# Optimization experiments

Hardware: AMD Instinct MI355X
Metric: run time of the kernel (lower is better)

## Reference

```python
import jax, jax.numpy as jnp
import numpy as np

DIM = 512
N = 131072


def _linear_params(key, dim):
    # torch nn.Linear default init: U(-1/sqrt(in), 1/sqrt(in)) for W and b
    kw, kb = jax.random.split(key)
    bound = 1.0 / np.sqrt(dim)
    W = jax.random.uniform(kw, (dim, dim), jnp.float32, -bound, bound)
    b = jax.random.uniform(kb, (dim,), jnp.float32, -bound, bound)
    return W, b


def setup_inputs() -> dict:
    key = jax.random.key(0)
    ks = jax.random.split(key, 8)
    x = jax.random.normal(ks[0], (N, DIM), jnp.float32)
    h = jax.random.normal(ks[1], (N, DIM), jnp.float32)
    W_rx, b_rx = _linear_params(ks[2], DIM)
    W_rh, b_rh = _linear_params(ks[3], DIM)
    W_zx, b_zx = _linear_params(ks[4], DIM)
    W_zh, b_zh = _linear_params(ks[5], DIM)
    W_nx, b_nx = _linear_params(ks[6], DIM)
    W_nh, b_nh = _linear_params(ks[7], DIM)
    return {
        "x": x, "h": h,
        "W_rx": W_rx, "b_rx": b_rx, "W_rh": W_rh, "b_rh": b_rh,
        "W_zx": W_zx, "b_zx": b_zx, "W_zh": W_zh, "b_zh": b_zh,
        "W_nx": W_nx, "b_nx": b_nx, "W_nh": W_nh, "b_nh": b_nh,
    }


def reference(x, h, W_rx, b_rx, W_rh, b_rh, W_zx, b_zx, W_zh, b_zh,
              W_nx, b_nx, W_nh, b_nh):
    # torch Linear: y = x @ W.T + b  (W stored [out, in])
    r = jax.nn.sigmoid(x @ W_rx.T + b_rx + h @ W_rh.T + b_rh)
    z = jax.nn.sigmoid(x @ W_zx.T + b_zx + h @ W_zh.T + b_zh)
    n = jnp.tanh(x @ W_nx.T + b_nx + (r * h) @ W_nh.T + b_nh)
    return (1.0 - z) * n + z * h
```

## Files before the change

kernel.cpp:

```cpp
#include <hip/hip_runtime.h>

#define DIM 512
#define NROWS 131072

typedef __attribute__((ext_vector_type(8))) __bf16 bf16x8;
typedef __attribute__((ext_vector_type(4))) float f32x4;

__device__ __forceinline__ unsigned short f2bf(float f) {
  unsigned u = __builtin_bit_cast(unsigned, f);
  return (unsigned short)((u + 0x7FFFu + ((u >> 16) & 1u)) >> 16);
}
__device__ __forceinline__ float bf2f(unsigned short u) {
  return __builtin_bit_cast(float, (unsigned)u << 16);
}

__device__ __forceinline__ f32x4 mfma16(bf16x8 a, bf16x8 b, f32x4 c) {
  return __builtin_amdgcn_mfma_f32_16x16x32_bf16(a, b, c, 0, 0, 0);
}

__device__ __forceinline__ float sigmoid_fast(float v) {
  return 1.0f / (1.0f + __expf(-v));
}
__device__ __forceinline__ float tanh_fast(float v) {
  float e = __expf(2.0f * v);
  return 1.0f - 2.0f / (e + 1.0f);
}

__global__ void prepack_weights(const float* __restrict__ W0, const float* __restrict__ W1,
                                const float* __restrict__ W2, const float* __restrict__ W3,
                                const float* __restrict__ W4, const float* __restrict__ W5,
                                unsigned short* __restrict__ out) {
  int idx = blockIdx.x * 256 + threadIdx.x;
  int e = idx & 7;
  int l = (idx >> 3) & 63;
  int c = (idx >> 9) & 31;
  int f = (idx >> 14) & 15;
  int g = idx >> 18;
  const float* W = (g == 0) ? W0 : (g == 1) ? W1 : (g == 2) ? W2
                 : (g == 3) ? W3 : (g == 4) ? W4 : W5;
  int row = c * 16 + (l & 15);
  int kk  = f * 32 + ((l >> 4) << 3) + e;
  out[idx] = f2bf(W[row * DIM + kk]);
}

__global__ void prep_x(const float* __restrict__ x, unsigned short* __restrict__ xb) {
  size_t i = (size_t)(blockIdx.x * 256 + threadIdx.x) * 8;
  float4 a0 = *(const float4*)(x + i);
  float4 a1 = *(const float4*)(x + i + 4);
  union { unsigned short us[8]; uint4 v; } p;
  p.us[0] = f2bf(a0.x); p.us[1] = f2bf(a0.y); p.us[2] = f2bf(a0.z); p.us[3] = f2bf(a0.w);
  p.us[4] = f2bf(a1.x); p.us[5] = f2bf(a1.y); p.us[6] = f2bf(a1.z); p.us[7] = f2bf(a1.w);
  *(uint4*)(xb + i) = p.v;
}

__global__ __launch_bounds__(512, 2)
void gru_fused(const float* __restrict__ h,
               const unsigned short* __restrict__ xb,
               const unsigned char* __restrict__ WB,
               const float* __restrict__ b_rx, const float* __restrict__ b_rh,
               const float* __restrict__ b_zx, const float* __restrict__ b_zh,
               const float* __restrict__ b_nx, const float* __restrict__ b_nh,
               float* __restrict__ out) {
  __shared__ __align__(1024) unsigned char lds[65536];

  const int tid  = threadIdx.x;
  const int lane = tid & 63;
  const int w    = tid >> 6;
  const int row0 = blockIdx.x * 64;
  const int lr   = lane & 15;
  const int lk   = lane >> 4;
  const int boff = w * 4096 + lane * 16;

  auto loadB = [&](int g, int f, bf16x8 (&b)[4]) {
    const unsigned char* p = WB + (((size_t)(g * 16 + f)) << 15) + boff;
#pragma unroll
    for (int cf = 0; cf < 4; ++cf)
      b[cf] = *(const bf16x8*)(p + cf * 1024);
  };
  auto loadXA = [&](int f, bf16x8 (&a)[4]) {
#pragma unroll
    for (int rf = 0; rf < 4; ++rf)
      a[rf] = *(const bf16x8*)(xb + (size_t)(row0 + rf * 16 + lr) * DIM
                               + f * 32 + lk * 8);
  };
  auto readLDS = [&](int f, bf16x8 (&a)[4]) {
#pragma unroll
    for (int rf = 0; rf < 4; ++rf)
      a[rf] = *(const bf16x8*)&lds[f * 4096 + rf * 1024 + lane * 16];
  };

#define WINDOW(Aset, Bset, ACC)                                                \
  _Pragma("unroll")                                                            \
  for (int rf_ = 0; rf_ < 4; ++rf_)                                            \
    _Pragma("unroll")                                                          \
    for (int cf_ = 0; cf_ < 4; ++cf_)                                          \
      ACC[rf_][cf_] = mfma16(Aset[rf_], Bset[cf_], ACC[rf_][cf_]);

  bf16x8 bA[4], bB[4], xaC[4], xaN[4], ha[4];

  loadB(0, 0, bA);
  loadB(1, 0, bB);
  loadXA(0, xaC);
#pragma unroll
  for (int it = 0; it < 16; ++it) {
    int i = tid + it * 512;
    int row = i >> 7;
    int k = (i & 127) * 4;
    float4 hv4 = *(const float4*)(h + (size_t)(row0 + row) * DIM + k);
    union { unsigned short us[4]; uint2 v; } p;
    p.us[0] = f2bf(hv4.x); p.us[1] = f2bf(hv4.y);
    p.us[2] = f2bf(hv4.z); p.us[3] = f2bf(hv4.w);
    *(uint2*)&lds[(k >> 5) * 4096 + (row >> 4) * 1024
                  + (((k >> 3) & 3) * 16 + (row & 15)) * 16 + (k & 4) * 2] = p.v;
  }
  __syncthreads();

  f32x4 accR[4][4] = {}, accZ[4][4] = {};
#pragma unroll 1
  for (int f = 0; f < 16; ++f) {
    const int fn = (f < 15) ? f + 1 : 15;
    readLDS(f, ha);
    WINDOW(xaC, bA, accR);
    loadB(2, f, bA);
    WINDOW(xaC, bB, accZ);
    loadB(3, f, bB);
    loadXA(fn, xaN);
    WINDOW(ha, bA, accR);
    loadB(0, fn, bA);
    WINDOW(ha, bB, accZ);
    loadB(1, fn, bB);
#pragma unroll
    for (int rf = 0; rf < 4; ++rf) xaC[rf] = xaN[rf];
  }

  loadB(4, 0, bA);
  loadB(5, 0, bB);
  loadXA(0, xaC);
  __syncthreads();

#pragma unroll
  for (int cf = 0; cf < 4; ++cf) {
    const int col  = (w * 4 + cf) * 16 + lr;
    const float bs = b_rx[col] + b_rh[col];
    const int fcol = col >> 5;
    const int l2b  = ((col >> 3) & 3) * 16;
    const int eb   = (col & 7) * 2;
#pragma unroll
    for (int rf = 0; rf < 4; ++rf) {
#pragma unroll
      for (int j = 0; j < 4; ++j) {
        const int rsub = lk * 4 + j;
        const int addr = fcol * 4096 + rf * 1024 + (l2b + rsub) * 16 + eb;
        unsigned short hu = *(const unsigned short*)&lds[addr];
        float rv = sigmoid_fast(accR[rf][cf][j] + bs);
        *(unsigned short*)&lds[addr] = f2bf(rv * bf2f(hu));
      }
    }
  }
  __syncthreads();

  f32x4 accN[4][4] = {};
#pragma unroll 1
  for (int f = 0; f < 16; ++f) {
    const int fn = (f < 15) ? f + 1 : 15;
    readLDS(f, ha);
    WINDOW(xaC, bA, accN);
    loadB(4, fn, bA);
    loadXA(fn, xaN);
    WINDOW(ha, bB, accN);
    loadB(5, fn, bB);
#pragma unroll
    for (int rf = 0; rf < 4; ++rf) xaC[rf] = xaN[rf];
  }

#pragma unroll
  for (int cf = 0; cf < 4; ++cf) {
    const int col  = (w * 4 + cf) * 16 + lr;
    const float bn = b_nx[col] + b_nh[col];
    const float bz = b_zx[col] + b_zh[col];
#pragma unroll
    for (int rf = 0; rf < 4; ++rf) {
#pragma unroll
      for (int j = 0; j < 4; ++j) {
        const int row = rf * 16 + lk * 4 + j;
        const size_t off = (size_t)(row0 + row) * DIM + col;
        float hv = h[off];
        float nv = tanh_fast(accN[rf][cf][j] + bn);
        float zv = sigmoid_fast(accZ[rf][cf][j] + bz);
        out[off] = (1.0f - zv) * nv + zv * hv;
      }
    }
  }
#undef WINDOW
}

extern "C" void kernel_launch(void* const* d_in, const int* in_sizes, int n_in,
                              void* d_out, int out_size, void* d_ws, size_t ws_size,
                              hipStream_t stream) {
  const float* x    = (const float*)d_in[0];
  const float* h    = (const float*)d_in[1];
  const float* W_rx = (const float*)d_in[2];
  const float* b_rx = (const float*)d_in[3];
  const float* W_rh = (const float*)d_in[4];
  const float* b_rh = (const float*)d_in[5];
  const float* W_zx = (const float*)d_in[6];
  const float* b_zx = (const float*)d_in[7];
  const float* W_zh = (const float*)d_in[8];
  const float* b_zh = (const float*)d_in[9];
  const float* W_nx = (const float*)d_in[10];
  const float* b_nx = (const float*)d_in[11];
  const float* W_nh = (const float*)d_in[12];
  const float* b_nh = (const float*)d_in[13];

  unsigned char* ws = (unsigned char*)d_ws;
  unsigned short* wpack = (unsigned short*)ws;
  unsigned short* xb    = (unsigned short*)(ws + (4ull << 20));

  prepack_weights<<<6144, 256, 0, stream>>>(W_rx, W_zx, W_rh, W_zh, W_nx, W_nh, wpack);
  prep_x<<<32768, 256, 0, stream>>>(x, xb);
  gru_fused<<<NROWS / 64, 512, 0, stream>>>(h, xb, (const unsigned char*)wpack,
                                            b_rx, b_rh, b_zx, b_zh, b_nx, b_nh,
                                            (float*)d_out);
}
```

Before: 726.2 us.

## Enlarge row tile to 128 and run gates as three sequential sweeps

The fused GRU kernel now handles 128 rows per block, with 8 waves in a 2x4 grid, each computing a 64x128 output tile. The r, z and n gates are computed in three separate sweeps that share one accumulator set, with z staged through the output buffer and r*h staged in a 128 KB LDS buffer. h is optionally pre-converted to bf16 in a separate pass, and each sweep wraps its MFMAs in s_setprio. The aim is more B-operand reuse per weight load and fewer live accumulators. The cost is that x and h are re-read across sweeps, z makes an extra round trip through global memory, and the larger LDS allocation limits blocks per CU.

```diff
diff --git a/kernel.cpp b/kernel.cpp
--- a/kernel.cpp
+++ b/kernel.cpp
@@ -2,6 +2,7 @@
 
 #define DIM 512
 #define NROWS 131072
+#define MB 128
 
 typedef __attribute__((ext_vector_type(8))) __bf16 bf16x8;
 typedef __attribute__((ext_vector_type(4))) float f32x4;
@@ -43,155 +44,172 @@
   out[idx] = f2bf(W[row * DIM + kk]);
 }
 
-__global__ void prep_x(const float* __restrict__ x, unsigned short* __restrict__ xb) {
+__global__ void prep_bf16(const float* __restrict__ in, unsigned short* __restrict__ ob) {
   size_t i = (size_t)(blockIdx.x * 256 + threadIdx.x) * 8;
-  float4 a0 = *(const float4*)(x + i);
-  float4 a1 = *(const float4*)(x + i + 4);
+  float4 a0 = *(const float4*)(in + i);
+  float4 a1 = *(const float4*)(in + i + 4);
   union { unsigned short us[8]; uint4 v; } p;
   p.us[0] = f2bf(a0.x); p.us[1] = f2bf(a0.y); p.us[2] = f2bf(a0.z); p.us[3] = f2bf(a0.w);
   p.us[4] = f2bf(a1.x); p.us[5] = f2bf(a1.y); p.us[6] = f2bf(a1.z); p.us[7] = f2bf(a1.w);
-  *(uint4*)(xb + i) = p.v;
+  *(uint4*)(ob + i) = p.v;
 }
 
 __global__ __launch_bounds__(512, 2)
-void gru_fused(const float* __restrict__ h,
+void gru_fused(const float* __restrict__ x, const float* __restrict__ h,
                const unsigned short* __restrict__ xb,
+               const unsigned short* __restrict__ hb,
                const unsigned char* __restrict__ WB,
                const float* __restrict__ b_rx, const float* __restrict__ b_rh,
                const float* __restrict__ b_zx, const float* __restrict__ b_zh,
                const float* __restrict__ b_nx, const float* __restrict__ b_nh,
                float* __restrict__ out) {
-  __shared__ __align__(1024) unsigned char lds[65536];
+  __shared__ __align__(1024) unsigned char lds[131072];
 
   const int tid  = threadIdx.x;
   const int lane = tid & 63;
   const int w    = tid >> 6;
-  const int row0 = blockIdx.x * 64;
+  const int wr   = w >> 2;
+  const int wc   = w & 3;
+  const int row0 = blockIdx.x * MB;
+  const int rb   = row0 + wr * 64;
   const int lr   = lane & 15;
   const int lk   = lane >> 4;
-  const int boff = w * 4096 + lane * 16;
-
-  auto loadB = [&](int g, int f, bf16x8 (&b)[4]) {
-    const unsigned char* p = WB + (((size_t)(g * 16 + f)) << 15) + boff;
-#pragma unroll
-    for (int cf = 0; cf < 4; ++cf)
+
+  bf16x8 bX[8], bH[8], axA[4], axB[4], ahC[4];
+  f32x4 acc[4][8];
+
+  auto loadB = [&](int g, int f, bf16x8 (&b)[8]) {
+    const unsigned char* p = WB + (((size_t)(g * 16 + f)) << 15)
+                             + (wc * 8) * 1024 + lane * 16;
+#pragma unroll
+    for (int cf = 0; cf < 8; ++cf)
       b[cf] = *(const bf16x8*)(p + cf * 1024);
   };
-  auto loadXA = [&](int f, bf16x8 (&a)[4]) {
+  auto loadA = [&](const unsigned short* bp, const float* fp, int f, bf16x8 (&a)[4]) {
+    if (bp) {
+#pragma unroll
+      for (int rf = 0; rf < 4; ++rf)
+        a[rf] = *(const bf16x8*)(bp + (size_t)(rb + rf * 16 + lr) * DIM
+                                 + f * 32 + lk * 8);
+    } else {
+#pragma unroll
+      for (int rf = 0; rf < 4; ++rf) {
+        const float* p = fp + (size_t)(rb + rf * 16 + lr) * DIM + f * 32 + lk * 8;
+        float4 u0 = *(const float4*)p;
+        float4 u1 = *(const float4*)(p + 4);
+        union { unsigned short us[8]; bf16x8 v; } c;
+        c.us[0]=f2bf(u0.x); c.us[1]=f2bf(u0.y); c.us[2]=f2bf(u0.z); c.us[3]=f2bf(u0.w);
+        c.us[4]=f2bf(u1.x); c.us[5]=f2bf(u1.y); c.us[6]=f2bf(u1.z); c.us[7]=f2bf(u1.w);
+        a[rf] = c.v;
+      }
+    }
+  };
+  auto readRH = [&](int f, bf16x8 (&a)[4]) {
 #pragma unroll
     for (int rf = 0; rf < 4; ++rf)
-      a[rf] = *(const bf16x8*)(xb + (size_t)(row0 + rf * 16 + lr) * DIM
-                               + f * 32 + lk * 8);
+      a[rf] = *(const bf16x8*)&lds[f * 8192 + (wr * 4 + rf) * 1024 + lane * 16];
   };
-  auto readLDS = [&](int f, bf16x8 (&a)[4]) {
+
+#define WIN(A, B)                                                              \
+  do {                                                                         \
+    __builtin_amdgcn_s_setprio(1);                                             \
+    _Pragma("unroll")                                                          \
+    for (int rf_ = 0; rf_ < 4; ++rf_)                                          \
+      _Pragma("unroll")                                                        \
+      for (int cf_ = 0; cf_ < 8; ++cf_)                                        \
+        acc[rf_][cf_] = mfma16(A[rf_], B[cf_], acc[rf_][cf_]);                 \
+    __builtin_amdgcn_s_setprio(0);                                             \
+  } while (0)
+
+#define LOADAH_G(F)  loadA(hb, h, (F), ahC)
+#define LOADAH_RH(F) readRH((F), ahC)
+
+#define SWEEP(GX, GH, AH)                                                      \
+  {                                                                            \
+    _Pragma("unroll")                                                          \
+    for (int rf_ = 0; rf_ < 4; ++rf_)                                          \
+      _Pragma("unroll")                                                        \
+      for (int cf_ = 0; cf_ < 8; ++cf_)                                        \
+        acc[rf_][cf_] = (f32x4){0.f, 0.f, 0.f, 0.f};                           \
+    loadB((GX), 0, bX); loadB((GH), 0, bH);                                    \
+    loadA(xb, x, 0, axA); AH(0);                                               \
+    _Pragma("unroll 1")                                                        \
+    for (int f2 = 0; f2 < 8; ++f2) {                                           \
+      {                                                                        \
+        const int f1 = 2 * f2 + 1;                                             \
+        loadA(xb, x, f1, axB);                                                 \
+        WIN(axA, bX); loadB((GX), f1, bX);                                     \
+        WIN(ahC, bH); loadB((GH), f1, bH); AH(f1);                             \
+      }                                                                        \
+      {                                                                        \
+        const int f1 = (f2 < 7) ? 2 * f2 + 2 : 15;                             \
+        loadA(xb, x, f1, axA);                                                 \
+        WIN(axB, bX); loadB((GX), f1, bX);                                     \
+        WIN(ahC, bH); loadB((GH), f1, bH); AH(f1);                             \
+      }                                                                        \
+    }                                                                          \
+  }
+
+  SWEEP(1, 3, LOADAH_G);
+#pragma unroll
+  for (int cf = 0; cf < 8; ++cf) {
+    const int col = wc * 128 + cf * 16 + lr;
+    const float bz = b_zx[col] + b_zh[col];
 #pragma unroll
     for (int rf = 0; rf < 4; ++rf)
-      a[rf] = *(const bf16x8*)&lds[f * 4096 + rf * 1024 + lane * 16];
-  };
-
-#define WINDOW(Aset, Bset, ACC)                                                \
-  _Pragma("unroll")                                                            \
-  for (int rf_ = 0; rf_ < 4; ++rf_)                                            \
-    _Pragma("unroll")                                                          \
-    for (int cf_ = 0; cf_ < 4; ++cf_)                                          \
-      ACC[rf_][cf_] = mfma16(Aset[rf_], Bset[cf_], ACC[rf_][cf_]);
-
-  bf16x8 bA[4], bB[4], xaC[4], xaN[4], ha[4];
-
-  loadB(0, 0, bA);
-  loadB(1, 0, bB);
-  loadXA(0, xaC);
-#pragma unroll
-  for (int it = 0; it < 16; ++it) {
-    int i = tid + it * 512;
-    int row = i >> 7;
-    int k = (i & 127) * 4;
-    float4 hv4 = *(const float4*)(h + (size_t)(row0 + row) * DIM + k);
-    union { unsigned short us[4]; uint2 v; } p;
-    p.us[0] = f2bf(hv4.x); p.us[1] = f2bf(hv4.y);
-    p.us[2] = f2bf(hv4.z); p.us[3] = f2bf(hv4.w);
-    *(uint2*)&lds[(k >> 5) * 4096 + (row >> 4) * 1024
-                  + (((k >> 3) & 3) * 16 + (row & 15)) * 16 + (k & 4) * 2] = p.v;
-  }
-  __syncthreads();
-
-  f32x4 accR[4][4] = {}, accZ[4][4] = {};
-#pragma unroll 1
-  for (int f = 0; f < 16; ++f) {
-    const int fn = (f < 15) ? f + 1 : 15;
-    readLDS(f, ha);
-    WINDOW(xaC, bA, accR);
-    loadB(2, f, bA);
-    WINDOW(xaC, bB, accZ);
-    loadB(3, f, bB);
-    loadXA(fn, xaN);
-    WINDOW(ha, bA, accR);
-    loadB(0, fn, bA);
-    WINDOW(ha, bB, accZ);
-    loadB(1, fn, bB);
-#pragma unroll
-    for (int rf = 0; rf < 4; ++rf) xaC[rf] = xaN[rf];
-  }
-
-  loadB(4, 0, bA);
-  loadB(5, 0, bB);
-  loadXA(0, xaC);
-  __syncthreads();
-
-#pragma unroll
-  for (int cf = 0; cf < 4; ++cf) {
-    const int col  = (w * 4 + cf) * 16 + lr;
+#pragma unroll
+      for (int j = 0; j < 4; ++j) {
+        const int row = rb + rf * 16 + lk * 4 + j;
+        out[(size_t)row * DIM + col] = sigmoid_fast(acc[rf][cf][j] + bz);
+      }
+  }
+
+  SWEEP(0, 2, LOADAH_G);
+#pragma unroll
+  for (int cf = 0; cf < 8; ++cf) {
+    const int col = wc * 128 + cf * 16 + lr;
     const float bs = b_rx[col] + b_rh[col];
-    const int fcol = col >> 5;
-    const int l2b  = ((col >> 3) & 3) * 16;
-    const int eb   = (col & 7) * 2;
+    const int fI  = col >> 5;
+    const int l2b = ((col >> 3) & 3) * 16;
+    const int eb  = (col & 7) * 2;
 #pragma unroll
     for (int rf = 0; rf < 4; ++rf) {
 #pragma unroll
       for (int j = 0; j < 4; ++j) {
         const int rsub = lk * 4 + j;
-        const int addr = fcol * 4096 + rf * 1024 + (l2b + rsub) * 16 + eb;
-        unsigned short hu = *(const unsigned short*)&lds[addr];
-        float rv = sigmoid_fast(accR[rf][cf][j] + bs);
-        *(unsigned short*)&lds[addr] = f2bf(rv * bf2f(hu));
+        const int row  = rb + rf * 16 + rsub;
+        const size_t off = (size_t)row * DIM + col;
+        float hv = hb ? bf2f(hb[off]) : h[off];
+        float rv = sigmoid_fast(acc[rf][cf][j] + bs);
+        *(unsigned short*)&lds[fI * 8192 + (wr * 4 + rf) * 1024
+                               + (l2b + rsub) * 16 + eb] = f2bf(rv * hv);
       }
     }
   }
   __syncthreads();
 
-  f32x4 accN[4][4] = {};
-#pragma unroll 1
-  for (int f = 0; f < 16; ++f) {
-    const int fn = (f < 15) ? f + 1 : 15;
-    readLDS(f, ha);
-    WINDOW(xaC, bA, accN);
-    loadB(4, fn, bA);
-    loadXA(fn, xaN);
-    WINDOW(ha, bB, accN);
-    loadB(5, fn, bB);
-#pragma unroll
-    for (int rf = 0; rf < 4; ++rf) xaC[rf] = xaN[rf];
-  }
-
-#pragma unroll
-  for (int cf = 0; cf < 4; ++cf) {
-    const int col  = (w * 4 + cf) * 16 + lr;
+  SWEEP(4, 5, LOADAH_RH);
+#pragma unroll
+  for (int cf = 0; cf < 8; ++cf) {
+    const int col = wc * 128 + cf * 16 + lr;
     const float bn = b_nx[col] + b_nh[col];
-    const float bz = b_zx[col] + b_zh[col];
 #pragma unroll
     for (int rf = 0; rf < 4; ++rf) {
 #pragma unroll
       for (int j = 0; j < 4; ++j) {
-        const int row = rf * 16 + lk * 4 + j;
-        const size_t off = (size_t)(row0 + row) * DIM + col;
+        const int row = rb + rf * 16 + lk * 4 + j;
+        const size_t off = (size_t)row * DIM + col;
+        float nv = tanh_fast(acc[rf][cf][j] + bn);
+        float zv = out[off];
         float hv = h[off];
-        float nv = tanh_fast(accN[rf][cf][j] + bn);
-        float zv = sigmoid_fast(accZ[rf][cf][j] + bz);
         out[off] = (1.0f - zv) * nv + zv * hv;
       }
     }
   }
-#undef WINDOW
+#undef SWEEP
+#undef WIN
+#undef LOADAH_G
+#undef LOADAH_RH
 }
 
 extern "C" void kernel_launch(void* const* d_in, const int* in_sizes, int n_in,
@@ -214,11 +232,20 @@
 
   unsigned char* ws = (unsigned char*)d_ws;
   unsigned short* wpack = (unsigned short*)ws;
-  unsigned short* xb    = (unsigned short*)(ws + (4ull << 20));
+  const size_t xb_off = 4ull << 20;
+  const size_t hb_off = xb_off + (size_t)NROWS * DIM * 2;
+  const size_t need_x = hb_off;
+  const size_t need_h = hb_off + (size_t)NROWS * DIM * 2;
+  unsigned short* xb = (ws_size >= need_x) ? (unsigned short*)(ws + xb_off)
+                                           : (unsigned short*)nullptr;
+  unsigned short* hb = (ws_size >= need_h) ? (unsigned short*)(ws + hb_off)
+                                           : (unsigned short*)nullptr;
 
   prepack_weights<<<6144, 256, 0, stream>>>(W_rx, W_zx, W_rh, W_zh, W_nx, W_nh, wpack);
-  prep_x<<<32768, 256, 0, stream>>>(x, xb);
-  gru_fused<<<NROWS / 64, 512, 0, stream>>>(h, xb, (const unsigned char*)wpack,
+  if (xb) prep_bf16<<<32768, 256, 0, stream>>>(x, xb);
+  if (hb) prep_bf16<<<32768, 256, 0, stream>>>(h, hb);
+  gru_fused<<<NROWS / MB, 512, 0, stream>>>(x, h, xb, hb,
+                                            (const unsigned char*)wpack,
                                             b_rx, b_rh, b_zx, b_zh, b_nx, b_nh,
                                             (float*)d_out);
 }
```

Result: slower. 2.234 ms (+207.6%).
